# Performance work log

Hardware: AMD Instinct MI355X
Metric: run time of the kernel (lower is better)

Reference implementation:

```python
import jax, jax.numpy as jnp
import numpy as np

NUM_HEADS = 8
D_MODEL = 128
MAX_LEN = 500  # RelativePositionalEncoding default


def setup_inputs() -> dict:
    key = jax.random.key(0)
    ks = jax.random.split(key, 13)
    B, S, D = 4, 1024, D_MODEL
    d = {
        'query': jax.random.normal(ks[0], (B, S, D), jnp.float32),
        'key': jax.random.normal(ks[1], (B, S, D), jnp.float32),
        'value': jax.random.normal(ks[2], (B, S, D), jnp.float32),
        # nn.Linear weights stored as (out, in), bias (out,)
        'Wq': jax.random.normal(ks[3], (D, D), jnp.float32) * 0.05,
        'bq': jax.random.normal(ks[4], (D,), jnp.float32) * 0.05,
        'Wk': jax.random.normal(ks[5], (D, D), jnp.float32) * 0.05,
        'bk': jax.random.normal(ks[6], (D,), jnp.float32) * 0.05,
        'Wv': jax.random.normal(ks[7], (D, D), jnp.float32) * 0.05,
        'bv': jax.random.normal(ks[8], (D,), jnp.float32) * 0.05,
        'Wo': jax.random.normal(ks[9], (D, D), jnp.float32) * 0.05,
        'bo': jax.random.normal(ks[10], (D,), jnp.float32) * 0.05,
        # embeddings_table: (2*max_len+1, d_model)
        'emb_table': jax.random.normal(ks[11], (2 * MAX_LEN + 1, D), jnp.float32) * 0.05,
    }
    return d


def reference(query, key, value, Wq, bq, Wk, bk, Wv, bv, Wo, bo, emb_table):
    B, S, D = query.shape
    H = NUM_HEADS
    hd = D // H

    def proj(x, W, b):
        # nn.Linear: x @ W.T + b, then split heads -> [B,H,S,hd]
        return (x @ W.T + b).reshape(B, S, H, hd).transpose(0, 2, 1, 3)

    Q = proj(query, Wq, bq)
    K = proj(key, Wk, bk)
    V = proj(value, Wv, bv)

    scores = jnp.einsum('bhqd,bhkd->bhqk', Q, K) / jnp.sqrt(jnp.float32(hd))

    # relative position bias: table gather (S,S,D) -> (S,S,H,hd);
    # batch dim of the torch expand is redundant, so contract directly.
    r = jnp.arange(S)
    rel_idx = jnp.clip(r[None, :] - r[:, None], -MAX_LEN, MAX_LEN) + MAX_LEN  # (S,S)
    E = emb_table[rel_idx].reshape(S, S, H, hd)  # (q,k,h,d)
    scores = scores + jnp.einsum('bhqd,qkhd->bhqk', Q, E)

    attn = jax.nn.softmax(scores + 1e-9, axis=-1)
    out = jnp.einsum('bhqk,bhkd->bhqd', attn, V)
    out = out.transpose(0, 2, 1, 3).reshape(B, S, D)
    return out @ Wo.T + bo
```

## Files before the change

### kernel.cpp

```cpp
#include <hip/hip_runtime.h>

#define NH 8
#define HD 16
#define SLEN 1024
#define BATCH 4
#define MAXL 500
#define NSEG 4
#define KTILES_PER_SEG 8

typedef float f32x4  __attribute__((ext_vector_type(4)));
typedef float f32x16 __attribute__((ext_vector_type(16)));
typedef short s16x8  __attribute__((ext_vector_type(8)));

__device__ inline ushort f2bf(float f) {
    uint u = __builtin_bit_cast(uint, f);
    u = (u + 0x7fffu + ((u >> 16) & 1u)) >> 16;
    return (ushort)u;
}
__device__ inline float bf2f(ushort h) {
    uint u = ((uint)h) << 16;
    return __builtin_bit_cast(float, u);
}

__global__ __launch_bounds__(256) void prep_bf16(
    const float* __restrict__ xq, const float* __restrict__ xk, const float* __restrict__ xv,
    const float* __restrict__ Wq, const float* __restrict__ Wk,
    const float* __restrict__ Wv, const float* __restrict__ Wo,
    const float* __restrict__ emb,
    ushort* __restrict__ xqb, ushort* __restrict__ xkb, ushort* __restrict__ xvb,
    ushort* __restrict__ wqb, ushort* __restrict__ wkb,
    ushort* __restrict__ wvb, ushort* __restrict__ wob,
    ushort* __restrict__ embb)
{
    const int XTOT = 3 * 524288;
    const int WTOT = 4 * 16384;
    const int ETOT = (2 * MAXL + 1) * 128;
    int e0 = (blockIdx.x * 256 + threadIdx.x) * 8;
    const float* src;
    ushort* dst;
    int off;
    if (e0 < XTOT) {
        int which = e0 >> 19; off = e0 & 524287;
        src = which == 0 ? xq : which == 1 ? xk : xv;
        dst = which == 0 ? xqb : which == 1 ? xkb : xvb;
    } else if (e0 < XTOT + WTOT) {
        int t = e0 - XTOT; int which = t >> 14; off = t & 16383;
        src = which == 0 ? Wq : which == 1 ? Wk : which == 2 ? Wv : Wo;
        dst = which == 0 ? wqb : which == 1 ? wkb : which == 2 ? wvb : wob;
    } else if (e0 < XTOT + WTOT + ETOT) {
        off = e0 - XTOT - WTOT; src = emb; dst = embb;
    } else {
        return;
    }
    const float4 a = *(const float4*)&src[off];
    const float4 b = *(const float4*)&src[off + 4];
    ushort tmp[8] = {f2bf(a.x), f2bf(a.y), f2bf(a.z), f2bf(a.w),
                     f2bf(b.x), f2bf(b.y), f2bf(b.z), f2bf(b.w)};
    *(s16x8*)&dst[off] = *(const s16x8*)tmp;
}

__global__ __launch_bounds__(64) void qkv_gemm(
    const ushort* __restrict__ xqb, const ushort* __restrict__ xkb, const ushort* __restrict__ xvb,
    const ushort* __restrict__ wqb, const ushort* __restrict__ wkb, const ushort* __restrict__ wvb,
    const float* __restrict__ bq, const float* __restrict__ bk, const float* __restrict__ bv,
    ushort* __restrict__ Qh, ushort* __restrict__ Kh, ushort* __restrict__ Vt)
{
    const int mode = blockIdx.y;
    const ushort* X = mode == 0 ? xqb : mode == 1 ? xkb : xvb;
    const ushort* W = mode == 0 ? wqb : mode == 1 ? wkb : wvb;
    const float* bb = mode == 0 ? bq : mode == 1 ? bk : bv;

    const int l = threadIdx.x;
    const int row = l & 15, kh = l >> 4;
    const int mt = blockIdx.x >> 2, nq = blockIdx.x & 3;
    const int m0 = mt * 32, n0 = nq * 32;

    s16x8 af[2][4], bfr[2][4];
    #pragma unroll
    for (int ms = 0; ms < 2; ++ms)
        #pragma unroll
        for (int ki = 0; ki < 4; ++ki)
            af[ms][ki] = *(const s16x8*)&X[(size_t)(m0 + 16*ms + row) * 128 + 32*ki + 8*kh];
    #pragma unroll
    for (int ns = 0; ns < 2; ++ns)
        #pragma unroll
        for (int ki = 0; ki < 4; ++ki)
            bfr[ns][ki] = *(const s16x8*)&W[(size_t)(n0 + 16*ns + row) * 128 + 32*ki + 8*kh];

    f32x4 acc[2][2];
    #pragma unroll
    for (int ms = 0; ms < 2; ++ms)
        #pragma unroll
        for (int ns = 0; ns < 2; ++ns)
            #pragma unroll
            for (int r = 0; r < 4; ++r) acc[ms][ns][r] = 0.f;

    #pragma unroll
    for (int ki = 0; ki < 4; ++ki)
        #pragma unroll
        for (int ms = 0; ms < 2; ++ms)
            #pragma unroll
            for (int ns = 0; ns < 2; ++ns)
                acc[ms][ns] = __builtin_amdgcn_mfma_f32_16x16x32_bf16(af[ms][ki], bfr[ns][ki], acc[ms][ns], 0, 0, 0);

    const float scale = (mode == 1) ? 0.25f : 1.0f;
    const int b = m0 >> 10;
    #pragma unroll
    for (int ns = 0; ns < 2; ++ns) {
        const int n = n0 + 16*ns + row;
        const int hh = n >> 4, d = n & 15;
        const float bias = bb[n];
        #pragma unroll
        for (int ms = 0; ms < 2; ++ms) {
            if (mode == 2) {
                ushort4 pk;
                pk.x = f2bf(acc[ms][ns][0] + bias);
                pk.y = f2bf(acc[ms][ns][1] + bias);
                pk.z = f2bf(acc[ms][ns][2] + bias);
                pk.w = f2bf(acc[ms][ns][3] + bias);
                const int s0 = (m0 & 1023) + 16*ms + kh * 4;
                *(ushort4*)&Vt[((size_t)((b*8 + hh)*16 + d)) * SLEN + s0] = pk;
            } else {
                ushort* dst = (mode == 0) ? Qh : Kh;
                #pragma unroll
                for (int r = 0; r < 4; ++r) {
                    const int mm = m0 + 16*ms + kh * 4 + r;
                    const int s = mm & 1023;
                    dst[((size_t)(b*8 + hh) * SLEN + s) * HD + d] = f2bf((acc[ms][ns][r] + bias) * scale);
                }
            }
        }
    }
}

__global__ __launch_bounds__(256) void attn_mfma(
    const ushort* __restrict__ Qh, const ushort* __restrict__ Kh,
    const ushort* __restrict__ Vtg, const ushort* __restrict__ emb_bf,
    float* __restrict__ mp, float* __restrict__ lp, float* __restrict__ op)
{
    __shared__ __align__(16) ushort Kt[32][24];
    __shared__ __align__(16) ushort Vt[16][40];
    __shared__ __align__(16) ushort Eb[160][24];
    __shared__ __align__(16) ushort Pl[4][32][40];
    __shared__ __align__(16) ushort Rl[4][64][36];
    __shared__ float scb[4][32];

    const int tid = threadIdx.x;
    const int wid = tid >> 6, lane = tid & 63;
    const int hi = lane >> 5, q = lane & 31;
    const int bh = blockIdx.y, h = bh & 7;
    const int q0b = blockIdx.x * 128;
    const int q0w = q0b + wid * 32;
    const int seg = blockIdx.z;

    const s16x8 qf = *(const s16x8*)&Qh[((size_t)bh * SLEN + q0w + q) * HD + 8 * hi];

    f32x4 o0, o1;
    #pragma unroll
    for (int r = 0; r < 4; ++r) { o0[r] = 0.f; o1[r] = 0.f; }
    float m = -1e30f, l = 0.f;

    for (int kt = seg * KTILES_PER_SEG; kt < (seg + 1) * KTILES_PER_SEG; ++kt) {
        const int k0 = kt * 32;
        __syncthreads();
        {
            int e = tid * 2, r = e >> 4, d0 = e & 15;
            *(ushort2*)&Kt[r][d0] = *(const ushort2*)&Kh[((size_t)bh * SLEN + k0 + r) * HD + d0];
        }
        {
            int d = tid >> 4, kk = (tid & 15) * 2;
            *(ushort2*)&Vt[d][kk] = *(const ushort2*)&Vtg[((size_t)(bh * 16 + d)) * SLEN + k0 + kk];
        }
        {
            const int relbase = k0 - q0b - 127;
            for (int e = tid; e < 160 * 2; e += 256) {
                int r = e >> 1, c8 = (e & 1) * 8;
                int rel = relbase + r;
                rel = rel < -MAXL ? -MAXL : (rel > MAXL ? MAXL : rel);
                *(s16x8*)&Eb[r][c8] =
                    *(const s16x8*)&emb_bf[(size_t)(rel + MAXL) * 128 + h * HD + c8];
            }
        }
        __syncthreads();

        const s16x8 kf = *(const s16x8*)&Kt[q][8 * hi];
        f32x16 sa;
        #pragma unroll
        for (int i = 0; i < 16; ++i) sa[i] = 0.f;
        sa = __builtin_amdgcn_mfma_f32_32x32x16_bf16(kf, qf, sa, 0, 0, 0);

        const int j0w = 96 - 32 * wid;
        #pragma unroll
        for (int st = 0; st < 2; ++st) {
            const s16x8 ef = *(const s16x8*)&Eb[j0w + 32 * st + q][8 * hi];
            f32x16 ra;
            #pragma unroll
            for (int i = 0; i < 16; ++i) ra[i] = 0.f;
            ra = __builtin_amdgcn_mfma_f32_32x32x16_bf16(qf, ef, ra, 0, 0, 0);
            #pragma unroll
            for (int g = 0; g < 4; ++g) {
                ushort4 pk;
                pk.x = f2bf(ra[4*g + 0]); pk.y = f2bf(ra[4*g + 1]);
                pk.z = f2bf(ra[4*g + 2]); pk.w = f2bf(ra[4*g + 3]);
                *(ushort4*)&Rl[wid][32*st + q][8*g + 4*hi] = pk;
            }
        }

        float p[16];
        float tm = -1e30f;
        #pragma unroll
        for (int r = 0; r < 16; ++r) {
            const int krow = (r & 3) + 8 * (r >> 2) + 4 * hi;
            const float bias = bf2f(Rl[wid][krow - q + 31][q]);
            const float s = sa[r] + bias;
            p[r] = s;
            tm = fmaxf(tm, s);
        }
        tm = fmaxf(tm, __shfl_xor(tm, 32));
        const float mn = fmaxf(m, tm);
        const float scf = __expf(m - mn);
        float ls = 0.f;
        #pragma unroll
        for (int r = 0; r < 16; ++r) { p[r] = __expf(p[r] - mn); ls += p[r]; }
        ls += __shfl_xor(ls, 32);
        l = l * scf + ls;
        m = mn;
        scb[wid][q] = scf;

        #pragma unroll
        for (int g = 0; g < 4; ++g) {
            ushort4 pk;
            pk.x = f2bf(p[4*g + 0]); pk.y = f2bf(p[4*g + 1]);
            pk.z = f2bf(p[4*g + 2]); pk.w = f2bf(p[4*g + 3]);
            *(ushort4*)&Pl[wid][q][8*g + 4*hi] = pk;
        }

        const s16x8 vf = *(const s16x8*)&Vt[lane & 15][8 * (lane >> 4)];
        {
            const s16x8 pa = *(const s16x8*)&Pl[wid][lane & 15][8 * (lane >> 4)];
            #pragma unroll
            for (int r = 0; r < 4; ++r) o0[r] *= scb[wid][(lane >> 4) * 4 + r];
            o0 = __builtin_amdgcn_mfma_f32_16x16x32_bf16(pa, vf, o0, 0, 0, 0);
        }
        {
            const s16x8 pa = *(const s16x8*)&Pl[wid][16 + (lane & 15)][8 * (lane >> 4)];
            #pragma unroll
            for (int r = 0; r < 4; ++r) o1[r] *= scb[wid][16 + (lane >> 4) * 4 + r];
            o1 = __builtin_amdgcn_mfma_f32_16x16x32_bf16(pa, vf, o1, 0, 0, 0);
        }
    }

    const size_t pbase = (size_t)(seg * 32 + bh) * SLEN;
    if (hi == 0) {
        mp[pbase + q0w + q] = m;
        lp[pbase + q0w + q] = l;
    }
    #pragma unroll
    for (int half = 0; half < 2; ++half) {
        #pragma unroll
        for (int r = 0; r < 4; ++r) {
            const int qp = half * 16 + (lane >> 4) * 4 + r;
            op[(pbase + q0w + qp) * HD + (lane & 15)] = (half ? o1[r] : o0[r]);
        }
    }
}

__global__ __launch_bounds__(256) void merge_kernel(
    const float* __restrict__ mp, const float* __restrict__ lp,
    const float* __restrict__ op, ushort* __restrict__ ohbf)
{
    const int idx = blockIdx.x * 256 + threadIdx.x;
    const int d = idx & 15;
    const int row = idx >> 4;
    const int bh = row >> 10, q = row & 1023;
    const int h = bh & 7, b = bh >> 3;

    float ms[NSEG];
    float M = -1e30f;
    #pragma unroll
    for (int s = 0; s < NSEG; ++s) {
        ms[s] = mp[(size_t)s * 32 * SLEN + row];
        M = fmaxf(M, ms[s]);
    }
    float L = 0.f, acc = 0.f;
    #pragma unroll
    for (int s = 0; s < NSEG; ++s) {
        const float w = __expf(ms[s] - M);
        L += lp[(size_t)s * 32 * SLEN + row] * w;
        acc += op[((size_t)s * 32 * SLEN + row) * HD + d] * w;
    }
    ohbf[((size_t)(b * SLEN + q)) * 128 + h * HD + d] = f2bf(acc / L);
}

__global__ __launch_bounds__(64) void out_gemm(
    const ushort* __restrict__ ohbf, const ushort* __restrict__ wob,
    const float* __restrict__ bo, float* __restrict__ out)
{
    const int l = threadIdx.x;
    const int row = l & 15, kh = l >> 4;
    const int mt = blockIdx.x >> 2, nq = blockIdx.x & 3;
    const int m0 = mt * 32, n0 = nq * 32;

    s16x8 af[2][4], bfr[2][4];
    #pragma unroll
    for (int ms = 0; ms < 2; ++ms)
        #pragma unroll
        for (int ki = 0; ki < 4; ++ki)
            af[ms][ki] = *(const s16x8*)&ohbf[(size_t)(m0 + 16*ms + row) * 128 + 32*ki + 8*kh];
    #pragma unroll
    for (int ns = 0; ns < 2; ++ns)
        #pragma unroll
        for (int ki = 0; ki < 4; ++ki)
            bfr[ns][ki] = *(const s16x8*)&wob[(size_t)(n0 + 16*ns + row) * 128 + 32*ki + 8*kh];

    f32x4 acc[2][2];
    #pragma unroll
    for (int ms = 0; ms < 2; ++ms)
        #pragma unroll
        for (int ns = 0; ns < 2; ++ns)
            #pragma unroll
            for (int r = 0; r < 4; ++r) acc[ms][ns][r] = 0.f;

    #pragma unroll
    for (int ki = 0; ki < 4; ++ki)
        #pragma unroll
        for (int ms = 0; ms < 2; ++ms)
            #pragma unroll
            for (int ns = 0; ns < 2; ++ns)
                acc[ms][ns] = __builtin_amdgcn_mfma_f32_16x16x32_bf16(af[ms][ki], bfr[ns][ki], acc[ms][ns], 0, 0, 0);

    #pragma unroll
    for (int ns = 0; ns < 2; ++ns) {
        const int n = n0 + 16*ns + row;
        const float bias = bo[n];
        #pragma unroll
        for (int ms = 0; ms < 2; ++ms)
            #pragma unroll
            for (int r = 0; r < 4; ++r) {
                const int mm = m0 + 16*ms + kh * 4 + r;
                out[(size_t)mm * 128 + n] = acc[ms][ns][r] + bias;
            }
    }
}

extern "C" void kernel_launch(void* const* d_in, const int* in_sizes, int n_in,
                              void* d_out, int out_size, void* d_ws, size_t ws_size,
                              hipStream_t stream)
{
    const float* query  = (const float*)d_in[0];
    const float* key_in = (const float*)d_in[1];
    const float* value  = (const float*)d_in[2];
    const float* Wq = (const float*)d_in[3];
    const float* bq = (const float*)d_in[4];
    const float* Wk = (const float*)d_in[5];
    const float* bk = (const float*)d_in[6];
    const float* Wv = (const float*)d_in[7];
    const float* bv = (const float*)d_in[8];
    const float* Wo = (const float*)d_in[9];
    const float* bo = (const float*)d_in[10];
    const float* emb = (const float*)d_in[11];
    float* out = (float*)d_out;

    const size_t TEN = (size_t)BATCH * NH * SLEN * HD;
    const size_t WE  = 16384;
    const size_t EE  = (size_t)(2 * MAXL + 1) * 128;
    const size_t ROWS = (size_t)32 * SLEN;

    ushort* qh   = (ushort*)d_ws;
    ushort* kh   = qh + TEN;
    ushort* vtg  = kh + TEN;
    ushort* xqb  = vtg + TEN;
    ushort* xkb  = xqb + TEN;
    ushort* xvb  = xkb + TEN;
    ushort* wqb  = xvb + TEN;
    ushort* wkb  = wqb + WE;
    ushort* wvb  = wkb + WE;
    ushort* wob  = wvb + WE;
    ushort* embb = wob + WE;
    ushort* ohbf = embb + EE;
    float*  mp   = (float*)(ohbf + TEN);
    float*  lp   = mp + NSEG * ROWS;
    float*  op   = lp + NSEG * ROWS;

    prep_bf16<<<863, 256, 0, stream>>>(query, key_in, value, Wq, Wk, Wv, Wo, emb,
                                       xqb, xkb, xvb, wqb, wkb, wvb, wob, embb);
    qkv_gemm<<<dim3(512, 3), 64, 0, stream>>>(xqb, xkb, xvb, wqb, wkb, wvb,
                                              bq, bk, bv, qh, kh, vtg);
    attn_mfma<<<dim3(8, 32, NSEG), 256, 0, stream>>>(qh, kh, vtg, embb, mp, lp, op);
    merge_kernel<<<(32 * SLEN * HD) / 256, 256, 0, stream>>>(mp, lp, op, ohbf);
    out_gemm<<<512, 64, 0, stream>>>(ohbf, wob, bo, out);
}
```

Before: 120.2 us.

## Drop LDS staging, skip clamped rel-bias tiles, keep P in registers for PV

The attention kernel now reads K, V and embedding fragments straight from global memory instead of staging them in shared memory, which removes the two block-wide barriers per key tile. Tiles whose relative offsets all fall in a clamped region get a precomputed per-query constant bias and skip the embedding MFMAs. When the 32x32x8 bf16 MFMA builtin exists, P stays in registers and feeds the PV product directly, avoiding the shared-memory round trip. The split-K segment count is doubled to expose more parallelism, at the cost of more partial results for the merge kernel to combine.

```diff
diff --git a/kernel.cpp b/kernel.cpp
--- a/kernel.cpp
+++ b/kernel.cpp
@@ -5,12 +5,22 @@
 #define SLEN 1024
 #define BATCH 4
 #define MAXL 500
-#define NSEG 4
-#define KTILES_PER_SEG 8
+#define NSEG 8
+#define KTILES_PER_SEG 4
 
 typedef float f32x4  __attribute__((ext_vector_type(4)));
 typedef float f32x16 __attribute__((ext_vector_type(16)));
 typedef short s16x8  __attribute__((ext_vector_type(8)));
+typedef short s16x4  __attribute__((ext_vector_type(4)));
+
+#if defined(__has_builtin)
+#if __has_builtin(__builtin_amdgcn_mfma_f32_32x32x8bf16_1k)
+#define HAS_PV_REG 1
+#endif
+#endif
+#ifndef HAS_PV_REG
+#define HAS_PV_REG 0
+#endif
 
 __device__ inline ushort f2bf(float f) {
     uint u = __builtin_bit_cast(uint, f);
@@ -138,12 +148,11 @@
     const ushort* __restrict__ Vtg, const ushort* __restrict__ emb_bf,
     float* __restrict__ mp, float* __restrict__ lp, float* __restrict__ op)
 {
-    __shared__ __align__(16) ushort Kt[32][24];
-    __shared__ __align__(16) ushort Vt[16][40];
-    __shared__ __align__(16) ushort Eb[160][24];
-    __shared__ __align__(16) ushort Pl[4][32][40];
     __shared__ __align__(16) ushort Rl[4][64][36];
     __shared__ float scb[4][32];
+#if !HAS_PV_REG
+    __shared__ __align__(16) ushort Pl[4][32][40];
+#endif
 
     const int tid = threadIdx.x;
     const int wid = tid >> 6, lane = tid & 63;
@@ -155,67 +164,76 @@
 
     const s16x8 qf = *(const s16x8*)&Qh[((size_t)bh * SLEN + q0w + q) * HD + 8 * hi];
 
+    float cq_hi = 0.f, cq_lo = 0.f;
+    {
+        const s16x8 ehi = *(const s16x8*)&emb_bf[(size_t)(2 * MAXL) * 128 + h * HD + 8 * hi];
+        const s16x8 elo = *(const s16x8*)&emb_bf[h * HD + 8 * hi];
+        #pragma unroll
+        for (int j = 0; j < 8; ++j) {
+            cq_hi += bf2f((ushort)qf[j]) * bf2f((ushort)ehi[j]);
+            cq_lo += bf2f((ushort)qf[j]) * bf2f((ushort)elo[j]);
+        }
+        cq_hi += __shfl_xor(cq_hi, 32);
+        cq_lo += __shfl_xor(cq_lo, 32);
+    }
+
+#if HAS_PV_REG
+    f32x16 acc;
+    #pragma unroll
+    for (int i = 0; i < 16; ++i) acc[i] = 0.f;
+#else
     f32x4 o0, o1;
     #pragma unroll
     for (int r = 0; r < 4; ++r) { o0[r] = 0.f; o1[r] = 0.f; }
+#endif
     float m = -1e30f, l = 0.f;
 
     for (int kt = seg * KTILES_PER_SEG; kt < (seg + 1) * KTILES_PER_SEG; ++kt) {
         const int k0 = kt * 32;
-        __syncthreads();
-        {
-            int e = tid * 2, r = e >> 4, d0 = e & 15;
-            *(ushort2*)&Kt[r][d0] = *(const ushort2*)&Kh[((size_t)bh * SLEN + k0 + r) * HD + d0];
-        }
-        {
-            int d = tid >> 4, kk = (tid & 15) * 2;
-            *(ushort2*)&Vt[d][kk] = *(const ushort2*)&Vtg[((size_t)(bh * 16 + d)) * SLEN + k0 + kk];
-        }
-        {
-            const int relbase = k0 - q0b - 127;
-            for (int e = tid; e < 160 * 2; e += 256) {
-                int r = e >> 1, c8 = (e & 1) * 8;
-                int rel = relbase + r;
-                rel = rel < -MAXL ? -MAXL : (rel > MAXL ? MAXL : rel);
-                *(s16x8*)&Eb[r][c8] =
-                    *(const s16x8*)&emb_bf[(size_t)(rel + MAXL) * 128 + h * HD + c8];
-            }
-        }
-        __syncthreads();
-
-        const s16x8 kf = *(const s16x8*)&Kt[q][8 * hi];
+        const int relbase = k0 - q0b - 127;
+        const bool clampHi = (relbase >= MAXL);
+        const bool clampLo = (relbase + 159 <= -MAXL);
+
+        const s16x8 kf = *(const s16x8*)&Kh[((size_t)bh * SLEN + k0 + q) * HD + 8 * hi];
         f32x16 sa;
         #pragma unroll
         for (int i = 0; i < 16; ++i) sa[i] = 0.f;
         sa = __builtin_amdgcn_mfma_f32_32x32x16_bf16(kf, qf, sa, 0, 0, 0);
 
-        const int j0w = 96 - 32 * wid;
-        #pragma unroll
-        for (int st = 0; st < 2; ++st) {
-            const s16x8 ef = *(const s16x8*)&Eb[j0w + 32 * st + q][8 * hi];
-            f32x16 ra;
-            #pragma unroll
-            for (int i = 0; i < 16; ++i) ra[i] = 0.f;
-            ra = __builtin_amdgcn_mfma_f32_32x32x16_bf16(qf, ef, ra, 0, 0, 0);
-            #pragma unroll
-            for (int g = 0; g < 4; ++g) {
-                ushort4 pk;
-                pk.x = f2bf(ra[4*g + 0]); pk.y = f2bf(ra[4*g + 1]);
-                pk.z = f2bf(ra[4*g + 2]); pk.w = f2bf(ra[4*g + 3]);
-                *(ushort4*)&Rl[wid][32*st + q][8*g + 4*hi] = pk;
+        float p[16];
+        if (!(clampHi || clampLo)) {
+            const int j0w = 96 - 32 * wid;
+            #pragma unroll
+            for (int st = 0; st < 2; ++st) {
+                int rel = relbase + j0w + 32 * st + q;
+                rel = rel < -MAXL ? -MAXL : (rel > MAXL ? MAXL : rel);
+                const s16x8 ef = *(const s16x8*)&emb_bf[(size_t)(rel + MAXL) * 128 + h * HD + 8 * hi];
+                f32x16 ra;
+                #pragma unroll
+                for (int i = 0; i < 16; ++i) ra[i] = 0.f;
+                ra = __builtin_amdgcn_mfma_f32_32x32x16_bf16(qf, ef, ra, 0, 0, 0);
+                #pragma unroll
+                for (int g = 0; g < 4; ++g) {
+                    ushort4 pk;
+                    pk.x = f2bf(ra[4*g + 0]); pk.y = f2bf(ra[4*g + 1]);
+                    pk.z = f2bf(ra[4*g + 2]); pk.w = f2bf(ra[4*g + 3]);
+                    *(ushort4*)&Rl[wid][32*st + q][8*g + 4*hi] = pk;
+                }
             }
-        }
-
-        float p[16];
+            #pragma unroll
+            for (int r = 0; r < 16; ++r) {
+                const int krow = (r & 3) + 8 * (r >> 2) + 4 * hi;
+                p[r] = sa[r] + bf2f(Rl[wid][krow - q + 31][q]);
+            }
+        } else {
+            const float cq = clampHi ? cq_hi : cq_lo;
+            #pragma unroll
+            for (int r = 0; r < 16; ++r) p[r] = sa[r] + cq;
+        }
+
         float tm = -1e30f;
         #pragma unroll
-        for (int r = 0; r < 16; ++r) {
-            const int krow = (r & 3) + 8 * (r >> 2) + 4 * hi;
-            const float bias = bf2f(Rl[wid][krow - q + 31][q]);
-            const float s = sa[r] + bias;
-            p[r] = s;
-            tm = fmaxf(tm, s);
-        }
+        for (int r = 0; r < 16; ++r) tm = fmaxf(tm, p[r]);
         tm = fmaxf(tm, __shfl_xor(tm, 32));
         const float mn = fmaxf(m, tm);
         const float scf = __expf(m - mn);
@@ -227,6 +245,21 @@
         m = mn;
         scb[wid][q] = scf;
 
+#if HAS_PV_REG
+        #pragma unroll
+        for (int r = 0; r < 16; ++r) acc[r] *= scb[wid][(r & 3) + 8 * (r >> 2) + 4 * hi];
+        const int d = lane & 15;
+        __builtin_amdgcn_s_setprio(1);
+        #pragma unroll
+        for (int s = 0; s < 4; ++s) {
+            ushort pk4[4] = {f2bf(p[4*s + 0]), f2bf(p[4*s + 1]),
+                             f2bf(p[4*s + 2]), f2bf(p[4*s + 3])};
+            const s16x4 ap = *(const s16x4*)pk4;
+            const s16x4 vb = *(const s16x4*)&Vtg[((size_t)(bh * 16 + d)) * SLEN + k0 + 8*s + 4*hi];
+            acc = __builtin_amdgcn_mfma_f32_32x32x8bf16_1k(ap, vb, acc, 0, 0, 0);
+        }
+        __builtin_amdgcn_s_setprio(0);
+#else
         #pragma unroll
         for (int g = 0; g < 4; ++g) {
             ushort4 pk;
@@ -234,8 +267,7 @@
             pk.z = f2bf(p[4*g + 2]); pk.w = f2bf(p[4*g + 3]);
             *(ushort4*)&Pl[wid][q][8*g + 4*hi] = pk;
         }
-
-        const s16x8 vf = *(const s16x8*)&Vt[lane & 15][8 * (lane >> 4)];
+        const s16x8 vf = *(const s16x8*)&Vtg[((size_t)(bh * 16 + (lane & 15))) * SLEN + k0 + 8 * (lane >> 4)];
         {
             const s16x8 pa = *(const s16x8*)&Pl[wid][lane & 15][8 * (lane >> 4)];
             #pragma unroll
@@ -248,6 +280,7 @@
             for (int r = 0; r < 4; ++r) o1[r] *= scb[wid][16 + (lane >> 4) * 4 + r];
             o1 = __builtin_amdgcn_mfma_f32_16x16x32_bf16(pa, vf, o1, 0, 0, 0);
         }
+#endif
     }
 
     const size_t pbase = (size_t)(seg * 32 + bh) * SLEN;
@@ -255,6 +288,16 @@
         mp[pbase + q0w + q] = m;
         lp[pbase + q0w + q] = l;
     }
+#if HAS_PV_REG
+    if ((lane & 31) < 16) {
+        const int d = lane & 31;
+        #pragma unroll
+        for (int r = 0; r < 16; ++r) {
+            const int qp = (r & 3) + 8 * (r >> 2) + 4 * hi;
+            op[(pbase + q0w + qp) * HD + d] = acc[r];
+        }
+    }
+#else
     #pragma unroll
     for (int half = 0; half < 2; ++half) {
         #pragma unroll
@@ -263,6 +306,7 @@
             op[(pbase + q0w + qp) * HD + (lane & 15)] = (half ? o1[r] : o0[r]);
         }
     }
+#endif
 }
 
 __global__ __launch_bounds__(256) void merge_kernel(
```

New measurement: 126.3 us. 1.05x slower.
